# Performance work log

Hardware: AMD Instinct MI355X
Metric: run time of the kernel (lower is better)

The kernel has to match this reference:

```python
import jax, jax.numpy as jnp
import numpy as np

LONG, LAT = 256, 256
N = LONG * LAT
BATCH = 64
OUT_DIM = 16 * 16


def _build_coo():
    # Faithful reproduction of the torch init loops (vectorized):
    # identity diagonal + 8-neighbor stencil entries for interior rows,
    # each (x,y) pair added in BOTH (x,y) and (y,x) directions.
    # torch sparse matmul on the uncoalesced COO sums duplicate entries,
    # so shared interior edges effectively get weight 2 -- the .at[].add
    # scatter below reproduces exactly that summation semantics.
    diag = np.arange(N, dtype=np.int64)
    centers = np.arange(LAT + 1, (LONG - 1) * LAT - 1, dtype=np.int64)
    offs = np.array([-1, 1, LAT, -LAT, LAT - 1, LAT + 1, -LAT - 1, -LAT + 1], dtype=np.int64)
    neigh = (centers[:, None] + offs[None, :]).ravel()
    crep = np.repeat(centers, 8)
    rows = np.concatenate([diag, crep, neigh]).astype(np.int32)
    cols = np.concatenate([diag, neigh, crep]).astype(np.int32)
    vals = np.ones(rows.shape[0], dtype=np.float32)
    return rows, cols, vals


def setup_inputs() -> dict:
    key = jax.random.key(0)
    k1, k2, k3 = jax.random.split(key, 3)
    rows, cols, vals = _build_coo()
    x = jax.random.normal(k1, (BATCH, LONG, LAT), dtype=jnp.float32)
    W = jax.random.normal(k2, (OUT_DIM, N), dtype=jnp.float32) * 0.02  # lin1.weight
    b = jax.random.normal(k3, (OUT_DIM,), dtype=jnp.float32) * 0.02   # lin1.bias
    return {
        "x": x,
        "W": W,
        "b": b,
        "rows": jnp.asarray(rows),
        "cols": jnp.asarray(cols),
        "vals": jnp.asarray(vals),
    }


def reference(x, W, b, rows, cols, vals):
    B = x.shape[0]
    xf = x.reshape(B, -1)                      # [B, N]
    gathered = xf[:, cols] * vals               # [B, E]
    h1 = jnp.zeros((B, xf.shape[1]), xf.dtype).at[:, rows].add(gathered)  # A @ xf.T, transposed
    h2 = h1 @ W.T + b                           # dense linear
    return h2
```

## Files before the change

### kernel.cpp

```cpp
#include <hip/hip_runtime.h>
#include <hip/hip_bf16.h>


#define MB    64
#define NOUT  256
#define KDIM  65536
#define NTOT  (MB * KDIM)
#define KSP   256
#define NCH   (KDIM / KSP)
#define OTOT  (MB * NOUT)
#define LSTR  272

typedef __attribute__((ext_vector_type(8))) short bf16x8;
typedef __attribute__((ext_vector_type(8))) unsigned short ushort8v;
typedef __attribute__((ext_vector_type(4))) float f32x4;

__device__ __forceinline__ ushort f2bf(float f) {
    __hip_bfloat16 h = __float2bfloat16(f);
    return *reinterpret_cast<ushort*>(&h);
}
__device__ __forceinline__ float bf2f(ushort u) {
    return __uint_as_float((unsigned)u << 16);
}

__device__ __forceinline__ ushort8v stencil8v(const float* __restrict__ x, int g) {
    const int i8 = g & (KDIM - 1);
    union Span { float4 v[4]; float f[16]; };
    Span u, c, d;
    #pragma unroll
    for (int q = 0; q < 4; ++q) {
        int bu = g - 260 + 4 * q; if (bu < 0) bu = 0;
        int bc = g - 4   + 4 * q; if (bc < 0) bc = 0; if (bc > NTOT - 4) bc = NTOT - 4;
        int bd = g + 252 + 4 * q; if (bd > NTOT - 4) bd = NTOT - 4;
        u.v[q] = *(const float4*)(x + bu);
        c.v[q] = *(const float4*)(x + bc);
        d.v[q] = *(const float4*)(x + bd);
    }
    ushort8v ov;
    if (i8 >= 520 && i8 <= 65008) {
        #pragma unroll
        for (int e = 0; e < 8; ++e) {
            float nb = c.f[3 + e] + c.f[5 + e]
                     + u.f[3 + e] + u.f[4 + e] + u.f[5 + e]
                     + d.f[3 + e] + d.f[4 + e] + d.f[5 + e];
            ov[e] = (short)f2bf(fmaf(2.0f, nb, c.f[4 + e]));
        }
    } else {
        #pragma unroll
        for (int e = 0; e < 8; ++e) {
            const int ii = i8 + e;
            const float ci = ((unsigned)(ii - 257) <= (65278u - 257u)) ? 1.0f : 0.0f;
            float s = c.f[4 + e];
            const int   doff[8] = {-1, 1, -257, -256, -255, 255, 256, 257};
            const float* src[8] = {&c.f[3 + e], &c.f[5 + e],
                                   &u.f[3 + e], &u.f[4 + e], &u.f[5 + e],
                                   &d.f[3 + e], &d.f[4 + e], &d.f[5 + e]};
            #pragma unroll
            for (int t = 0; t < 8; ++t) {
                const int j = ii + doff[t];
                const float cj = ((unsigned)(j - 257) <= (65278u - 257u)) ? 1.0f : 0.0f;
                s = fmaf(ci + cj, *src[t], s);
            }
            ov[e] = (short)f2bf(s);
        }
    }
    return ov;
}

__global__ __launch_bounds__(1024, 4) void fused_sg(const float* __restrict__ x,
                                                    const float* __restrict__ W,
                                                    ushort* __restrict__ part) {
    __shared__ ushort hs[MB * LSTR];
    const int b  = blockIdx.x;
    const int kp = (b & 7) * 32 + (b >> 3);
    const int t  = threadIdx.x;

    {
        const int m = t >> 4;
        const int j = t & 15;
        const int g = m * KDIM + kp * KSP + j * 16;
        ushort8v o0 = stencil8v(x, g);
        ushort8v o1 = stencil8v(x, g + 8);
        *(ushort8v*)&hs[m * LSTR + j * 16]     = o0;
        *(ushort8v*)&hs[m * LSTR + j * 16 + 8] = o1;
    }
    __syncthreads();

    const int nt = t >> 6;
    const int l  = t & 63;
    const int lr = l & 15;
    const int lg = l >> 4;

    f32x4 acc[4];
    #pragma unroll
    for (int a = 0; a < 4; ++a) acc[a] = (f32x4){0.f, 0.f, 0.f, 0.f};

    const float* wp = W + (size_t)(nt * 16 + lr) * KDIM + kp * KSP + lg * 8;

    #pragma unroll
    for (int ks = 0; ks < KSP / 32; ++ks) {
        float4 w0 = *(const float4*)(wp + ks * 32);
        float4 w1 = *(const float4*)(wp + ks * 32 + 4);
        bf16x8 afrag[4];
        #pragma unroll
        for (int mt = 0; mt < 4; ++mt)
            afrag[mt] = *(const bf16x8*)&hs[(mt * 16 + lr) * LSTR + lg * 8 + ks * 32];
        union { ushort u[8]; bf16x8 v; } bb;
        bb.u[0] = f2bf(w0.x); bb.u[1] = f2bf(w0.y);
        bb.u[2] = f2bf(w0.z); bb.u[3] = f2bf(w0.w);
        bb.u[4] = f2bf(w1.x); bb.u[5] = f2bf(w1.y);
        bb.u[6] = f2bf(w1.z); bb.u[7] = f2bf(w1.w);
        #pragma unroll
        for (int mt = 0; mt < 4; ++mt)
            acc[mt] = __builtin_amdgcn_mfma_f32_16x16x32_bf16(afrag[mt], bb.v,
                                                              acc[mt], 0, 0, 0);
    }

    ushort* pb = part + (size_t)kp * OTOT + (size_t)(nt * 16 + lr) * MB;
    #pragma unroll
    for (int mt = 0; mt < 4; ++mt) {
        ushort4 s;
        s.x = f2bf(acc[mt][0]); s.y = f2bf(acc[mt][1]);
        s.z = f2bf(acc[mt][2]); s.w = f2bf(acc[mt][3]);
        *(ushort4*)(pb + mt * 16 + lg * 4) = s;
    }
}

__global__ __launch_bounds__(256) void reduce_bf16(const ushort* __restrict__ part,
                                                   const float* __restrict__ bias,
                                                   float* __restrict__ out) {
    __shared__ float red[256];
    const int ol = threadIdx.x & 31;
    const int cg = threadIdx.x >> 5;
    const int o  = blockIdx.x * 32 + ol;
    const ushort* p = part + (size_t)cg * 32 * OTOT + o;
    float s0 = 0.f, s1 = 0.f, s2 = 0.f, s3 = 0.f;
    #pragma unroll 2
    for (int i = 0; i < 32; i += 4) {
        s0 += bf2f(p[(size_t)(i + 0) * OTOT]);
        s1 += bf2f(p[(size_t)(i + 1) * OTOT]);
        s2 += bf2f(p[(size_t)(i + 2) * OTOT]);
        s3 += bf2f(p[(size_t)(i + 3) * OTOT]);
    }
    red[threadIdx.x] = (s0 + s1) + (s2 + s3);
    __syncthreads();
    if (cg == 0) {
        float v = red[ol];
        #pragma unroll
        for (int jj = 1; jj < 8; ++jj) v += red[jj * 32 + ol];
        const int n = o >> 6, m = o & 63;
        out[m * NOUT + n] = v + bias[n];
    }
}

extern "C" void kernel_launch(void* const* d_in, const int* in_sizes, int n_in,
                              void* d_out, int out_size, void* d_ws, size_t ws_size,
                              hipStream_t stream) {
    const float* x    = (const float*)d_in[0];
    const float* W    = (const float*)d_in[1];
    const float* bias = (const float*)d_in[2];
    float* out = (float*)d_out;

    ushort* part = (ushort*)d_ws;

    fused_sg<<<NCH, 1024, 0, stream>>>(x, W, part);
    reduce_bf16<<<OTOT / 32, 256, 0, stream>>>(part, bias, out);
}
```

Baseline: 33.92 us.

## Halve K split per block, give each wave two N tiles, prefetch W into registers

Halves the K slice per block to 128, so there are 512 blocks of 512 threads, and each wave now computes two 16-wide output tiles that reuse the same LDS A fragments. All W values for the slice are loaded into registers up front rather than inside the MFMA loop. The aim is more blocks, better A-fragment reuse and earlier issue of the W loads. In exchange it doubles the number of partial-sum slabs, so the reduce kernel reads twice as much data, and it raises register pressure.

Result: slower. 39.65 us (+16.9%).

```diff
diff --git a/kernel.cpp b/kernel.cpp
--- a/kernel.cpp
+++ b/kernel.cpp
@@ -6,10 +6,10 @@
 #define NOUT  256
 #define KDIM  65536
 #define NTOT  (MB * KDIM)
-#define KSP   256
+#define KSP   128
 #define NCH   (KDIM / KSP)
 #define OTOT  (MB * NOUT)
-#define LSTR  272
+#define LSTR  136
 
 typedef __attribute__((ext_vector_type(8))) short bf16x8;
 typedef __attribute__((ext_vector_type(8))) unsigned short ushort8v;
@@ -67,17 +67,17 @@
     return ov;
 }
 
-__global__ __launch_bounds__(1024, 4) void fused_sg(const float* __restrict__ x,
-                                                    const float* __restrict__ W,
-                                                    ushort* __restrict__ part) {
+__global__ __launch_bounds__(512, 4) void fused_sg(const float* __restrict__ x,
+                                                   const float* __restrict__ W,
+                                                   ushort* __restrict__ part) {
     __shared__ ushort hs[MB * LSTR];
     const int b  = blockIdx.x;
-    const int kp = (b & 7) * 32 + (b >> 3);
+    const int kp = (b & 7) * 64 + (b >> 3);
     const int t  = threadIdx.x;
 
     {
-        const int m = t >> 4;
-        const int j = t & 15;
+        const int m = t >> 3;
+        const int j = t & 7;
         const int g = m * KDIM + kp * KSP + j * 16;
         ushort8v o0 = stencil8v(x, g);
         ushort8v o1 = stencil8v(x, g + 8);
@@ -86,43 +86,66 @@
     }
     __syncthreads();
 
-    const int nt = t >> 6;
-    const int l  = t & 63;
-    const int lr = l & 15;
-    const int lg = l >> 4;
+    const int wid = t >> 6;
+    const int l   = t & 63;
+    const int lr  = l & 15;
+    const int lg  = l >> 4;
+    const int nt0 = wid * 2;
 
-    f32x4 acc[4];
+    const float* wp0 = W + (size_t)(nt0 * 16 + lr) * KDIM + kp * KSP + lg * 8;
+    const float* wp1 = wp0 + (size_t)16 * KDIM;
+
+    float4 wr0[8], wr1[8];
     #pragma unroll
-    for (int a = 0; a < 4; ++a) acc[a] = (f32x4){0.f, 0.f, 0.f, 0.f};
+    for (int q = 0; q < 4; ++q) {
+        wr0[2 * q]     = *(const float4*)(wp0 + q * 32);
+        wr0[2 * q + 1] = *(const float4*)(wp0 + q * 32 + 4);
+        wr1[2 * q]     = *(const float4*)(wp1 + q * 32);
+        wr1[2 * q + 1] = *(const float4*)(wp1 + q * 32 + 4);
+    }
 
-    const float* wp = W + (size_t)(nt * 16 + lr) * KDIM + kp * KSP + lg * 8;
+    f32x4 acc0[4], acc1[4];
+    #pragma unroll
+    for (int a = 0; a < 4; ++a) {
+        acc0[a] = (f32x4){0.f, 0.f, 0.f, 0.f};
+        acc1[a] = (f32x4){0.f, 0.f, 0.f, 0.f};
+    }
 
     #pragma unroll
     for (int ks = 0; ks < KSP / 32; ++ks) {
-        float4 w0 = *(const float4*)(wp + ks * 32);
-        float4 w1 = *(const float4*)(wp + ks * 32 + 4);
-        bf16x8 afrag[4];
+        bf16x8 af[4];
         #pragma unroll
         for (int mt = 0; mt < 4; ++mt)
-            afrag[mt] = *(const bf16x8*)&hs[(mt * 16 + lr) * LSTR + lg * 8 + ks * 32];
-        union { ushort u[8]; bf16x8 v; } bb;
-        bb.u[0] = f2bf(w0.x); bb.u[1] = f2bf(w0.y);
-        bb.u[2] = f2bf(w0.z); bb.u[3] = f2bf(w0.w);
-        bb.u[4] = f2bf(w1.x); bb.u[5] = f2bf(w1.y);
-        bb.u[6] = f2bf(w1.z); bb.u[7] = f2bf(w1.w);
+            af[mt] = *(const bf16x8*)&hs[(mt * 16 + lr) * LSTR + lg * 8 + ks * 32];
+        union { ushort u[8]; bf16x8 v; } b0, b1;
+        #pragma unroll
+        for (int e = 0; e < 4; ++e) {
+            b0.u[e]     = f2bf(wr0[2 * ks][e]);
+            b0.u[4 + e] = f2bf(wr0[2 * ks + 1][e]);
+            b1.u[e]     = f2bf(wr1[2 * ks][e]);
+            b1.u[4 + e] = f2bf(wr1[2 * ks + 1][e]);
+        }
         #pragma unroll
         for (int mt = 0; mt < 4; ++mt)
-            acc[mt] = __builtin_amdgcn_mfma_f32_16x16x32_bf16(afrag[mt], bb.v,
-                                                              acc[mt], 0, 0, 0);
+            acc0[mt] = __builtin_amdgcn_mfma_f32_16x16x32_bf16(af[mt], b0.v,
+                                                               acc0[mt], 0, 0, 0);
+        #pragma unroll
+        for (int mt = 0; mt < 4; ++mt)
+            acc1[mt] = __builtin_amdgcn_mfma_f32_16x16x32_bf16(af[mt], b1.v,
+                                                               acc1[mt], 0, 0, 0);
     }
 
-    ushort* pb = part + (size_t)kp * OTOT + (size_t)(nt * 16 + lr) * MB;
+    ushort* pb0 = part + (size_t)kp * OTOT + (size_t)(nt0 * 16 + lr) * MB;
+    ushort* pb1 = pb0 + (size_t)16 * MB;
     #pragma unroll
     for (int mt = 0; mt < 4; ++mt) {
-        ushort4 s;
-        s.x = f2bf(acc[mt][0]); s.y = f2bf(acc[mt][1]);
-        s.z = f2bf(acc[mt][2]); s.w = f2bf(acc[mt][3]);
-        *(ushort4*)(pb + mt * 16 + lg * 4) = s;
+        ushort4 s0, s1;
+        s0.x = f2bf(acc0[mt][0]); s0.y = f2bf(acc0[mt][1]);
+        s0.z = f2bf(acc0[mt][2]); s0.w = f2bf(acc0[mt][3]);
+        s1.x = f2bf(acc1[mt][0]); s1.y = f2bf(acc1[mt][1]);
+        s1.z = f2bf(acc1[mt][2]); s1.w = f2bf(acc1[mt][3]);
+        *(ushort4*)(pb0 + mt * 16 + lg * 4) = s0;
+        *(ushort4*)(pb1 + mt * 16 + lg * 4) = s1;
     }
 }
 
@@ -133,10 +156,10 @@
     const int ol = threadIdx.x & 31;
     const int cg = threadIdx.x >> 5;
     const int o  = blockIdx.x * 32 + ol;
-    const ushort* p = part + (size_t)cg * 32 * OTOT + o;
+    const ushort* p = part + (size_t)cg * 64 * OTOT + o;
     float s0 = 0.f, s1 = 0.f, s2 = 0.f, s3 = 0.f;
-    #pragma unroll 2
-    for (int i = 0; i < 32; i += 4) {
+    #pragma unroll 4
+    for (int i = 0; i < 64; i += 4) {
         s0 += bf2f(p[(size_t)(i + 0) * OTOT]);
         s1 += bf2f(p[(size_t)(i + 1) * OTOT]);
         s2 += bf2f(p[(size_t)(i + 2) * OTOT]);
@@ -163,6 +186,6 @@
 
     ushort* part = (ushort*)d_ws;
 
-    fused_sg<<<NCH, 1024, 0, stream>>>(x, W, part);
+    fused_sg<<<NCH, 512, 0, stream>>>(x, W, part);
     reduce_bf16<<<OTOT / 32, 256, 0, stream>>>(part, bias, out);
 }
```
